# Kernel optimization log

Hardware: AMD Instinct MI355X
Metric: run time of the kernel (lower is better)

Reference implementation:

```python
import jax, jax.numpy as jnp
import numpy as np

STRIDE = 1
PAD_INIT = 0


def _im2col(x, k, stride, padding):
    # torch.nn.functional.unfold equivalent: channel order (C, kh, kw), row-major spatial
    patches = jax.lax.conv_general_dilated_patches(
        x, (k, k), (stride, stride), [(padding, padding), (padding, padding)])
    # patches: (N, C*k*k, h_out, w_out)
    N, d, ho, wo = patches.shape
    # match torch code: view(N, d, L').permute(1,2,0).reshape(d, L'*N)
    X_col = patches.reshape(N, d, ho * wo).transpose(1, 2, 0).reshape(d, ho * wo * N)
    return X_col, ho, wo


def setup_inputs() -> dict:
    key = jax.random.key(0)
    k1, k2 = jax.random.split(key)
    x = jax.random.normal(k1, (32, 128, 28, 28), dtype=jnp.float32)
    W = jax.random.normal(k2, (128, 128, 3, 3), dtype=jnp.float32)
    return {"x": x, "W": W}


def reference(x, W):
    F_, C, kh, kw = W.shape
    N, _, H, _ = x.shape
    # 'full' conv output size per the module's formula
    h_out = (H - 1) * STRIDE - 2 * PAD_INIT + (kh - 1) + 1
    pad = ((h_out - 1) * STRIDE + kh - H) // 2
    X_col, ho, wo = _im2col(x, kh, STRIDE, pad)          # (d, L), d=C*k*k, L=ho*wo*N
    W_col = W.reshape(F_, -1)                            # (F, d)
    # intended quadratic 'adder' decomposition: out[f,l] = -0.5*||W_f - X_l||^2
    # = W_f . X_l - 0.5*||W_f||^2 - 0.5*||X_l||^2  (fused GEMM form, no (F,d,L) blowup)
    out = (W_col @ X_col
           - 0.5 * jnp.sum(W_col * W_col, axis=1)[:, None]
           - 0.5 * jnp.sum(X_col * X_col, axis=0)[None, :])  # (F, L)
    out = out.reshape(F_, ho, wo, N).transpose(3, 0, 1, 2)   # (N, F, ho, wo)
    return out
```

## Files before the change

kernel.cpp:

```cpp
#include <hip/hip_runtime.h>
#include <hip/hip_bf16.h>
#include <stdint.h>


#define N_IMG 32
#define C_IN 128
#define H_IN 28
#define HO 30
#define P_SP 900
#define F_OUT 128
#define K_TOT 1152

#define BLT 60
#define TPI 15
#define NBLK (N_IMG*TPI)
#define NSTEP 18

typedef __attribute__((ext_vector_type(8))) short bf16x8;
typedef __attribute__((ext_vector_type(4))) unsigned short u16x4;
typedef __attribute__((ext_vector_type(8))) unsigned short u16x8;
typedef __attribute__((ext_vector_type(4))) float f32x4;

__device__ __forceinline__ unsigned short f2bf(float f) {
  union { float f; unsigned u; } t; t.f = f;
  unsigned r = t.u + 0x7fffu + ((t.u >> 16) & 1u);
  return (unsigned short)(r >> 16);
}

__global__ void prep_w_kernel(const float* __restrict__ W,
                              unsigned short* __restrict__ Wbf,
                              float* __restrict__ wnorm) {
  int f = blockIdx.x;
  const float* Wf = W + f * K_TOT;
  float part = 0.f;
  for (int k = threadIdx.x; k < K_TOT; k += 256) {
    float v = Wf[k];
    part += v * v;
    int ch = k / 9, rr = k - ch * 9;
    Wbf[f * K_TOT + rr * 128 + ch] = f2bf(v);
  }
  __shared__ float red[256];
  red[threadIdx.x] = part;
  __syncthreads();
  for (int st = 128; st > 0; st >>= 1) {
    if (threadIdx.x < st) red[threadIdx.x] += red[threadIdx.x + st];
    __syncthreads();
  }
  if (threadIdx.x == 0) wnorm[f] = 0.5f * red[0];
}

__global__ __launch_bounds__(256, 2) void adder_fused_kernel(
    const float* __restrict__ x,
    const unsigned short* __restrict__ Wbf,
    const float* __restrict__ wnorm,
    float* __restrict__ out) {
  __shared__ unsigned short xfoot[128 * 128];
  __shared__ unsigned short A_lds[2][64 * 128];
  __shared__ float pixsum_s[128];
  __shared__ float xn_s[64];
  __shared__ float wn_s[F_OUT];

  int tid = threadIdx.x, lane = tid & 63, wid = tid >> 6;
  int bid = blockIdx.x;
  int n = bid / TPI, timg = bid - n * TPI;
  int i0 = timg * 2, p0 = timg * BLT;

  char* XF = (char*)xfoot;
  char* A0 = (char*)&A_lds[0][0];
  char* A1 = (char*)&A_lds[1][0];
  const char* WbfB = (const char*)Wbf;

  int kb = ((lane & 7) * 16) ^ ((lane >> 3) << 4);
  int a_goff[4];
#pragma unroll
  for (int a = 0; a < 4; a++) {
    int q = a * 4 + wid;
    int rowf = q * 8 + (lane >> 3);
    a_goff[a] = rowf * (K_TOT * 2) + kb;
  }
  int a_loff = wid * 1024 + lane * 16;

  auto STAGE = [&](int t, char* AB) {
    int off = t * 128;
#pragma unroll
    for (int a = 0; a < 4; a++)
      __builtin_amdgcn_global_load_lds(
          (const __attribute__((address_space(1))) void*)(WbfB + a_goff[a] + off),
          (__attribute__((address_space(3))) void*)(AB + a * 4096 + a_loff), 16, 0, 0);
  };

  STAGE(0, A0);
  if (tid < F_OUT) wn_s[tid] = wnorm[tid];

  for (int u = tid; u < 896; u += 256) {
    int r = u / 224, rem = u - r * 224;
    int w4 = rem >> 5, cq = rem & 31, c = cq * 4;
    int hr = i0 - 2 + r;
    float vv[4][4];
    if (hr >= 0 && hr < H_IN) {
#pragma unroll
      for (int q = 0; q < 4; q++) {
        float4 t4 = *(const float4*)(x + (((n * C_IN + c + q) * H_IN + hr) * H_IN + w4 * 4));
        vv[q][0] = t4.x; vv[q][1] = t4.y; vv[q][2] = t4.z; vv[q][3] = t4.w;
      }
    } else {
#pragma unroll
      for (int q = 0; q < 4; q++)
#pragma unroll
        for (int ws2 = 0; ws2 < 4; ws2++) vv[q][ws2] = 0.f;
    }
#pragma unroll
    for (int ws2 = 0; ws2 < 4; ws2++) {
      int wp = w4 * 4 + ws2 + 2;
      int pix = r * 32 + wp;
      u16x4 o;
#pragma unroll
      for (int q = 0; q < 4; q++) o[q] = f2bf(vv[q][ws2]);
      *(u16x4*)(XF + pix * 256 + ((c * 2) ^ ((pix & 15) << 4))) = o;
    }
  }
  {
    int r = tid >> 6, wi = (tid >> 4) & 3, slot = tid & 15;
    int wp = (wi < 2) ? wi : 28 + wi;
    int pix = r * 32 + wp;
    u16x8 z;
#pragma unroll
    for (int q = 0; q < 8; q++) z[q] = 0;
    *(u16x8*)(XF + pix * 256 + ((slot * 16) ^ ((pix & 15) << 4))) = z;
  }
  __syncthreads();

  {
    int pix = tid >> 1, ch = tid & 1;
    float ssum = 0.f;
#pragma unroll
    for (int q = 0; q < 8; q++) {
      u16x8 v8 = *(const u16x8*)(XF + pix * 256 + (((ch * 128) + q * 16) ^ ((pix & 15) << 4)));
#pragma unroll
      for (int e = 0; e < 8; e++) {
        union { unsigned u; float f; } cv; cv.u = ((unsigned)v8[e]) << 16;
        ssum += cv.f * cv.f;
      }
    }
    ssum += __shfl_xor(ssum, 1);
    if (!ch) pixsum_s[pix] = ssum;
  }
  __syncthreads();
  if (tid < BLT) {
    int il = tid / HO, j = tid - il * HO;
    float a9 = 0.f;
#pragma unroll
    for (int dh = 0; dh < 3; dh++)
#pragma unroll
      for (int dw = 0; dw < 3; dw++)
        a9 += pixsum_s[(il + dh) * 32 + (j + dw)];
    xn_s[tid] = 0.5f * a9;
  }
  __syncthreads();

  f32x4 acc[4][2];
#pragma unroll
  for (int mi = 0; mi < 4; mi++)
#pragma unroll
    for (int ni = 0; ni < 2; ni++)
      acc[mi][ni] = (f32x4){0.f, 0.f, 0.f, 0.f};

  int wr = wid >> 1, wc = wid & 1;
  int pix0[2];
#pragma unroll
  for (int ni = 0; ni < 2; ni++) {
    int cc = wc * 32 + ni * 16 + (lane & 15);
    if (cc > BLT - 1) cc = BLT - 1;
    int il = cc / HO, j = cc - il * HO;
    pix0[ni] = il * 32 + j;
  }
  int kfrag = (lane >> 4) * 16;

#pragma unroll 2
  for (int t = 0; t < NSTEP; t++) {
    char* ABc = (t & 1) ? A1 : A0;
    char* ABn = (t & 1) ? A0 : A1;
    if (t + 1 < NSTEP) STAGE(t + 1, ABn);

    int rr = t >> 1, half = t & 1;
    int dh = rr / 3, dw = rr - 3 * dh;
    int pofs = dh * 32 + dw;
    int bbase = half * 128;
#pragma unroll
    for (int kc = 0; kc < 2; kc++) {
      bf16x8 af[4], bfv[2];
#pragma unroll
      for (int mi = 0; mi < 4; mi++) {
        int rowf = wr * 64 + mi * 16 + (lane & 15);
        af[mi] = *(const bf16x8*)(ABc + rowf * 128 + ((kc * 64 + kfrag) ^ ((rowf & 7) << 4)));
      }
#pragma unroll
      for (int ni = 0; ni < 2; ni++) {
        int pix = pix0[ni] + pofs;
        bfv[ni] = *(const bf16x8*)(XF + pix * 256 + ((bbase + kc * 64 + kfrag) ^ ((pix & 15) << 4)));
      }
      __builtin_amdgcn_s_setprio(1);
#pragma unroll
      for (int mi = 0; mi < 4; mi++)
#pragma unroll
        for (int ni = 0; ni < 2; ni++)
          acc[mi][ni] = __builtin_amdgcn_mfma_f32_16x16x32_bf16(
              af[mi], bfv[ni], acc[mi][ni], 0, 0, 0);
      __builtin_amdgcn_s_setprio(0);
    }
    asm volatile("s_waitcnt vmcnt(0)" ::: "memory");
    __builtin_amdgcn_s_barrier();
  }

#pragma unroll
  for (int ni = 0; ni < 2; ni++) {
    int cc = wc * 32 + ni * 16 + (lane & 15);
    if (cc < BLT) {
      float xn = xn_s[cc];
      float* ob = out + (size_t)n * (F_OUT * P_SP) + p0 + cc;
#pragma unroll
      for (int mi = 0; mi < 4; mi++) {
        int f0 = wr * 64 + mi * 16 + (lane >> 4) * 4;
#pragma unroll
        for (int r2 = 0; r2 < 4; r2++) {
          int f = f0 + r2;
          ob[f * P_SP] = acc[mi][ni][r2] - wn_s[f] - xn;
        }
      }
    }
  }
}

extern "C" void kernel_launch(void* const* d_in, const int* in_sizes, int n_in,
                              void* d_out, int out_size, void* d_ws, size_t ws_size,
                              hipStream_t stream) {
  const float* x = (const float*)d_in[0];
  const float* W = (const float*)d_in[1];
  float* out = (float*)d_out;

  char* ws = (char*)d_ws;
  unsigned short* Wbf = (unsigned short*)(ws);
  float* wnorm = (float*)(ws + 294912);

  prep_w_kernel<<<F_OUT, 256, 0, stream>>>(W, Wbf, wnorm);
  adder_fused_kernel<<<NBLK, 256, 0, stream>>>(x, Wbf, wnorm, out);
}
```

Measured before the change: 29.58 us.

## Shrink weight staging tiles, raise occupancy, and stage output through LDS

```diff
diff --git a/kernel.cpp b/kernel.cpp
--- a/kernel.cpp
+++ b/kernel.cpp
@@ -6,6 +6,7 @@
 #define N_IMG 32
 #define C_IN 128
 #define H_IN 28
+#define HP 32
 #define HO 30
 #define P_SP 900
 #define F_OUT 128
@@ -14,7 +15,7 @@
 #define BLT 60
 #define TPI 15
 #define NBLK (N_IMG*TPI)
-#define NSTEP 18
+#define NSTEP 36
 
 typedef __attribute__((ext_vector_type(8))) short bf16x8;
 typedef __attribute__((ext_vector_type(4))) unsigned short u16x4;
@@ -49,15 +50,15 @@
   if (threadIdx.x == 0) wnorm[f] = 0.5f * red[0];
 }
 
-__global__ __launch_bounds__(256, 2) void adder_fused_kernel(
+__global__ __launch_bounds__(256, 3) void adder_fused_kernel(
     const float* __restrict__ x,
     const unsigned short* __restrict__ Wbf,
     const float* __restrict__ wnorm,
     float* __restrict__ out) {
   __shared__ unsigned short xfoot[128 * 128];
-  __shared__ unsigned short A_lds[2][64 * 128];
+  __shared__ unsigned short A_lds[2][128 * 32];
   __shared__ float pixsum_s[128];
-  __shared__ float xn_s[64];
+  __shared__ float xn_s[BLT];
   __shared__ float wn_s[F_OUT];
 
   int tid = threadIdx.x, lane = tid & 63, wid = tid >> 6;
@@ -66,30 +67,29 @@
   int i0 = timg * 2, p0 = timg * BLT;
 
   char* XF = (char*)xfoot;
-  char* A0 = (char*)&A_lds[0][0];
-  char* A1 = (char*)&A_lds[1][0];
   const char* WbfB = (const char*)Wbf;
 
-  int kb = ((lane & 7) * 16) ^ ((lane >> 3) << 4);
-  int a_goff[4];
-#pragma unroll
-  for (int a = 0; a < 4; a++) {
+  int kbl = (((lane & 3) ^ ((lane >> 2) & 3)) << 4);
+  int a_goff[2], a_loff[2];
+#pragma unroll
+  for (int a = 0; a < 2; a++) {
     int q = a * 4 + wid;
-    int rowf = q * 8 + (lane >> 3);
-    a_goff[a] = rowf * (K_TOT * 2) + kb;
-  }
-  int a_loff = wid * 1024 + lane * 16;
-
-  auto STAGE = [&](int t, char* AB) {
-    int off = t * 128;
-#pragma unroll
-    for (int a = 0; a < 4; a++)
+    int row = q * 16 + (lane >> 2);
+    a_goff[a] = row * (K_TOT * 2) + kbl;
+    a_loff[a] = q * 1024 + lane * 16;
+  }
+
+  auto STAGE = [&](int rr, int qt, int bufi) {
+    int off = rr * 256 + qt * 64;
+    char* AB = (char*)(&A_lds[bufi][0]);
+#pragma unroll
+    for (int a = 0; a < 2; a++)
       __builtin_amdgcn_global_load_lds(
           (const __attribute__((address_space(1))) void*)(WbfB + a_goff[a] + off),
-          (__attribute__((address_space(3))) void*)(AB + a * 4096 + a_loff), 16, 0, 0);
+          (__attribute__((address_space(3))) void*)(AB + a_loff[a]), 16, 0, 0);
   };
 
-  STAGE(0, A0);
+  STAGE(0, 0, 0);
   if (tid < F_OUT) wn_s[tid] = wnorm[tid];
 
   for (int u = tid; u < 896; u += 256) {
@@ -107,15 +107,15 @@
 #pragma unroll
       for (int q = 0; q < 4; q++)
 #pragma unroll
-        for (int ws2 = 0; ws2 < 4; ws2++) vv[q][ws2] = 0.f;
-    }
-#pragma unroll
-    for (int ws2 = 0; ws2 < 4; ws2++) {
-      int wp = w4 * 4 + ws2 + 2;
+        for (int e = 0; e < 4; e++) vv[q][e] = 0.f;
+    }
+#pragma unroll
+    for (int e = 0; e < 4; e++) {
+      int wp = w4 * 4 + e + 2;
       int pix = r * 32 + wp;
       u16x4 o;
 #pragma unroll
-      for (int q = 0; q < 4; q++) o[q] = f2bf(vv[q][ws2]);
+      for (int q = 0; q < 4; q++) o[q] = f2bf(vv[q][e]);
       *(u16x4*)(XF + pix * 256 + ((c * 2) ^ ((pix & 15) << 4))) = o;
     }
   }
@@ -166,38 +166,44 @@
       acc[mi][ni] = (f32x4){0.f, 0.f, 0.f, 0.f};
 
   int wr = wid >> 1, wc = wid & 1;
+  int colc = lane & 15, kg = lane >> 4;
   int pix0[2];
 #pragma unroll
   for (int ni = 0; ni < 2; ni++) {
-    int cc = wc * 32 + ni * 16 + (lane & 15);
+    int cc = wc * 32 + ni * 16 + colc;
     if (cc > BLT - 1) cc = BLT - 1;
     int il = cc / HO, j = cc - il * HO;
     pix0[ni] = il * 32 + j;
   }
-  int kfrag = (lane >> 4) * 16;
-
-#pragma unroll 2
-  for (int t = 0; t < NSTEP; t++) {
-    char* ABc = (t & 1) ? A1 : A0;
-    char* ABn = (t & 1) ? A0 : A1;
-    if (t + 1 < NSTEP) STAGE(t + 1, ABn);
-
-    int rr = t >> 1, half = t & 1;
-    int dh = rr / 3, dw = rr - 3 * dh;
-    int pofs = dh * 32 + dw;
-    int bbase = half * 128;
-#pragma unroll
-    for (int kc = 0; kc < 2; kc++) {
+  int asw = (colc & 3) << 4;
+
+  for (int rr2 = 0; rr2 < 9; rr2++) {
+#pragma unroll 4
+    for (int qt = 0; qt < 4; qt++) {
+      int t = rr2 * 4 + qt;
+      int cur = qt & 1;
+      if (t + 1 < NSTEP) {
+        int rn = (qt == 3) ? rr2 + 1 : rr2, qn = (qt + 1) & 3;
+        STAGE(rn, qn, cur ^ 1);
+        asm volatile("s_waitcnt vmcnt(2)" ::: "memory");
+      } else {
+        asm volatile("s_waitcnt vmcnt(0)" ::: "memory");
+      }
+      __builtin_amdgcn_s_barrier();
+
+      const char* AB = (const char*)(&A_lds[cur][0]);
+      int dh = rr2 / 3, dw = rr2 - 3 * dh;
+      int pofs = dh * 32 + dw;
       bf16x8 af[4], bfv[2];
 #pragma unroll
       for (int mi = 0; mi < 4; mi++) {
-        int rowf = wr * 64 + mi * 16 + (lane & 15);
-        af[mi] = *(const bf16x8*)(ABc + rowf * 128 + ((kc * 64 + kfrag) ^ ((rowf & 7) << 4)));
+        int row = wr * 64 + mi * 16 + colc;
+        af[mi] = *(const bf16x8*)(AB + row * 64 + ((kg * 16) ^ asw));
       }
 #pragma unroll
       for (int ni = 0; ni < 2; ni++) {
         int pix = pix0[ni] + pofs;
-        bfv[ni] = *(const bf16x8*)(XF + pix * 256 + ((bbase + kc * 64 + kfrag) ^ ((pix & 15) << 4)));
+        bfv[ni] = *(const bf16x8*)(XF + pix * 256 + ((qt * 64 + kg * 16) ^ ((pix & 15) << 4)));
       }
       __builtin_amdgcn_s_setprio(1);
 #pragma unroll
@@ -207,25 +213,32 @@
           acc[mi][ni] = __builtin_amdgcn_mfma_f32_16x16x32_bf16(
               af[mi], bfv[ni], acc[mi][ni], 0, 0, 0);
       __builtin_amdgcn_s_setprio(0);
-    }
-    asm volatile("s_waitcnt vmcnt(0)" ::: "memory");
-    __builtin_amdgcn_s_barrier();
-  }
-
-#pragma unroll
-  for (int ni = 0; ni < 2; ni++) {
-    int cc = wc * 32 + ni * 16 + (lane & 15);
-    if (cc < BLT) {
-      float xn = xn_s[cc];
-      float* ob = out + (size_t)n * (F_OUT * P_SP) + p0 + cc;
-#pragma unroll
-      for (int mi = 0; mi < 4; mi++) {
-        int f0 = wr * 64 + mi * 16 + (lane >> 4) * 4;
-#pragma unroll
-        for (int r2 = 0; r2 < 4; r2++) {
-          int f = f0 + r2;
-          ob[f * P_SP] = acc[mi][ni][r2] - wn_s[f] - xn;
-        }
+      __builtin_amdgcn_s_barrier();
+    }
+  }
+
+  float* Cst = (float*)xfoot;
+#pragma unroll
+  for (int mi = 0; mi < 4; mi++) {
+    int f0 = wr * 64 + mi * 16 + kg * 4;
+#pragma unroll
+    for (int ni = 0; ni < 2; ni++) {
+      int cc = wc * 32 + ni * 16 + colc;
+#pragma unroll
+      for (int r = 0; r < 4; r++)
+        Cst[(f0 + r) * 64 + cc] = acc[mi][ni][r];
+    }
+  }
+  __syncthreads();
+  {
+    int col = tid & 63, fq = tid >> 6;
+    if (col < BLT) {
+      float xn = xn_s[col];
+      float* ob = out + (size_t)n * (F_OUT * P_SP) + p0 + col;
+#pragma unroll
+      for (int q = 0; q < 32; q++) {
+        int f = fq * 32 + q;
+        __builtin_nontemporal_store(Cst[f * 64 + col] - wn_s[f] - xn, ob + f * P_SP);
       }
     }
   }
```

New measurement: 33.37 us. 12.8% more time.
